# Kernel tuning notes

Measured on AMD Instinct MI355X. Metric: run time of the kernel, lower is better.

The kernel has to match this reference:

```python
import jax, jax.numpy as jnp
import numpy as np

EPS_COS = 1e-8   # torch cosine_similarity eps
EPS_SHARP = 1e-6 # sharpening normalizer eps
SHIFT_RANGE = 3
MEM_WIDTH = 64


def setup_inputs() -> dict:
    key = jax.random.key(0)
    k1, k2, k3, k4, k5 = jax.random.split(key, 5)
    B, H, N, W, D = 64, 4, 16384, MEM_WIDTH, 1024
    P = W + 6  # key(W) + beta + gate + shift(3) + gamma
    return {
        "controller_state": jax.random.normal(k1, (B, D), dtype=jnp.float32),
        "prev_weights": jax.random.uniform(k2, (B, H, N), dtype=jnp.float32),
        "memory": jax.random.normal(k3, (B, N, W), dtype=jnp.float32),
        "W_read": jax.random.normal(k4, (P * H, D), dtype=jnp.float32) * 0.02,
        "b_read": jax.random.normal(k5, (P * H,), dtype=jnp.float32) * 0.02,
    }


def reference(controller_state, prev_weights, memory, W_read, b_read):
    B, H, N = prev_weights.shape
    Wd = MEM_WIDTH
    # read head parameters: [B, H, P]
    params = (controller_state @ W_read.T + b_read).reshape(B, H, -1)
    key = params[..., :Wd]                                   # [B,H,W]
    beta = jax.nn.softplus(params[..., Wd])                  # [B,H]
    gate = jax.nn.sigmoid(params[..., Wd + 1])               # [B,H]
    shift = jax.nn.softmax(params[..., Wd + 2:Wd + 2 + SHIFT_RANGE], axis=-1)  # [B,H,3]
    gamma = 1.0 + jax.nn.softplus(params[..., Wd + 2 + SHIFT_RANGE])           # [B,H]

    # content addressing: cosine similarity of key vs each memory slot
    dots = jnp.einsum('bhw,bnw->bhn', key, memory)           # [B,H,N]
    key_norm = jnp.maximum(jnp.linalg.norm(key, axis=-1), EPS_COS)        # [B,H]
    mem_norm = jnp.maximum(jnp.linalg.norm(memory, axis=-1), EPS_COS)     # [B,N]
    sim = dots / (key_norm[:, :, None] * mem_norm[:, None, :])
    content_w = jax.nn.softmax(sim * beta[:, :, None], axis=-1)           # [B,H,N]

    # interpolate with previous weights
    g = gate[:, :, None]
    gated = g * content_w + (1.0 - g) * prev_weights                     # [B,H,N]

    # circular shift: out[pos] = s0*w[pos-1] + s1*w[pos] + s2*w[pos+1]
    shifted = (shift[..., 0:1] * jnp.roll(gated, 1, axis=-1)
               + shift[..., 1:2] * gated
               + shift[..., 2:3] * jnp.roll(gated, -1, axis=-1))

    # sharpening
    sharp = shifted ** gamma[:, :, None]
    sharp = sharp / (jnp.sum(sharp, axis=-1, keepdims=True) + EPS_SHARP)
    return sharp  # [B,H,N]
```

## Files before the change

kernel.cpp:

```cpp
#include <hip/hip_runtime.h>
#include <math.h>

#define B  64
#define H  4
#define NN 16384
#define WD 64
#define DD 1024
#define PP 70

typedef float fx4 __attribute__((ext_vector_type(4)));

__device__ __forceinline__ float softplus_f(float x) {
    return fmaxf(x, 0.f) + log1pf(expf(-fabsf(x)));
}

__global__ __launch_bounds__(256) void k_params(
    const float* __restrict__ state, const float* __restrict__ Wr,
    const float* __restrict__ br, float* __restrict__ kscaled,
    float* __restrict__ coef)
{
    int bh = blockIdx.x;
    int b  = bh >> 2, h = bh & 3;
    int tid = threadIdx.x, wave = tid >> 6, lane = tid & 63;
    __shared__ float sp[PP];
    __shared__ float sbc[1];

    const float4* st4 = (const float4*)(state + (size_t)b * DD);
    for (int j = wave; j < PP; j += 4) {
        const float4* w4 = (const float4*)(Wr + (size_t)(h * PP + j) * DD);
        float acc = 0.f;
        #pragma unroll
        for (int q = 0; q < 4; ++q) {
            float4 wv = w4[lane + 64 * q];
            float4 sv = st4[lane + 64 * q];
            acc += wv.x * sv.x + wv.y * sv.y + wv.z * sv.z + wv.w * sv.w;
        }
        #pragma unroll
        for (int m = 32; m >= 1; m >>= 1) acc += __shfl_xor(acc, m, 64);
        if (lane == 0) sp[j] = acc + br[h * PP + j];
    }
    __syncthreads();
    if (tid == 0) {
        float ss = 0.f;
        for (int w = 0; w < WD; ++w) ss += sp[w] * sp[w];
        float knorm = fmaxf(sqrtf(ss), 1e-8f);
        float beta  = softplus_f(sp[64]);
        float gate  = 1.f / (1.f + expf(-sp[65]));
        float m3 = fmaxf(sp[66], fmaxf(sp[67], sp[68]));
        float e0 = expf(sp[66] - m3), e1 = expf(sp[67] - m3), e2 = expf(sp[68] - m3);
        float es = e0 + e1 + e2;
        float gamma = 1.f + softplus_f(sp[69]);
        float* c = coef + bh * 8;
        c[0] = gate; c[1] = e0 / es; c[2] = e1 / es; c[3] = e2 / es; c[4] = gamma;
        sbc[0] = beta / knorm;
    }
    __syncthreads();
    if (tid < WD) kscaled[bh * WD + tid] = sp[tid] * sbc[0];
}

__global__ __launch_bounds__(256) void k_sim(
    const float* __restrict__ mem, const float* __restrict__ kscaled,
    float* __restrict__ sbuf)
{
    int tid = threadIdx.x, wave = tid >> 6, lane = tid & 63;
    int blk = blockIdx.x;
    int b = blk >> 8;
    int nblk = (blk & 255) * 64;
    int r = lane >> 3, c = lane & 7;

    const float* ksb = kscaled + b * 4 * WD + c * 8;
    float4 k0a = *(const float4*)(ksb + 0 * WD);
    float4 k0b = *(const float4*)(ksb + 0 * WD + 4);
    float4 k1a = *(const float4*)(ksb + 1 * WD);
    float4 k1b = *(const float4*)(ksb + 1 * WD + 4);
    float4 k2a = *(const float4*)(ksb + 2 * WD);
    float4 k2b = *(const float4*)(ksb + 2 * WD + 4);
    float4 k3a = *(const float4*)(ksb + 3 * WD);
    float4 k3b = *(const float4*)(ksb + 3 * WD + 4);

    int nw = nblk + wave * 16;
    #pragma unroll
    for (int it = 0; it < 2; ++it) {
        int n = nw + it * 8 + r;
        const fx4* rp = (const fx4*)(mem + ((size_t)b * NN + n) * WD + c * 8);
        fx4 v0 = __builtin_nontemporal_load(rp);
        fx4 v1 = __builtin_nontemporal_load(rp + 1);
        float d0 = v0.x*k0a.x + v0.y*k0a.y + v0.z*k0a.z + v0.w*k0a.w
                 + v1.x*k0b.x + v1.y*k0b.y + v1.z*k0b.z + v1.w*k0b.w;
        float d1 = v0.x*k1a.x + v0.y*k1a.y + v0.z*k1a.z + v0.w*k1a.w
                 + v1.x*k1b.x + v1.y*k1b.y + v1.z*k1b.z + v1.w*k1b.w;
        float d2 = v0.x*k2a.x + v0.y*k2a.y + v0.z*k2a.z + v0.w*k2a.w
                 + v1.x*k2b.x + v1.y*k2b.y + v1.z*k2b.z + v1.w*k2b.w;
        float d3 = v0.x*k3a.x + v0.y*k3a.y + v0.z*k3a.z + v0.w*k3a.w
                 + v1.x*k3b.x + v1.y*k3b.y + v1.z*k3b.z + v1.w*k3b.w;
        float q  = v0.x*v0.x + v0.y*v0.y + v0.z*v0.z + v0.w*v0.w
                 + v1.x*v1.x + v1.y*v1.y + v1.z*v1.z + v1.w*v1.w;
        #pragma unroll
        for (int m = 1; m < 8; m <<= 1) {
            d0 += __shfl_xor(d0, m, 64);
            d1 += __shfl_xor(d1, m, 64);
            d2 += __shfl_xor(d2, m, 64);
            d3 += __shfl_xor(d3, m, 64);
            q  += __shfl_xor(q,  m, 64);
        }
        if (c < 4) {
            float mn = fmaxf(sqrtf(q), 1e-8f);
            float d  = (c == 0) ? d0 : ((c == 1) ? d1 : ((c == 2) ? d2 : d3));
            sbuf[((size_t)(b * 4 + c)) * NN + n] = d / mn;
        }
    }
}

__global__ __launch_bounds__(1024) void k_head(
    const float* __restrict__ sbuf, const float* __restrict__ prev,
    const float* __restrict__ coef, float* __restrict__ out)
{
    __shared__ float lds[NN];
    int bh = blockIdx.x;
    int tid = threadIdx.x, wave = tid >> 6, lane = tid & 63;
    const float* srow = sbuf + (size_t)bh * NN;
    const float* prow = prev + (size_t)bh * NN;
    float* orow = out + (size_t)bh * NN;
    const float* c = coef + bh * 8;
    float gate = c[0], sh0 = c[1], sh1 = c[2], sh2 = c[3], gamma = c[4];

    float sv[16], pw[16];
    #pragma unroll
    for (int k = 0; k < 16; ++k) {
        sv[k] = srow[tid + k * 1024];
        pw[k] = prow[tid + k * 1024];
    }
    float m = sv[0];
    #pragma unroll
    for (int k = 1; k < 16; ++k) m = fmaxf(m, sv[k]);
    #pragma unroll
    for (int d = 32; d >= 1; d >>= 1) m = fmaxf(m, __shfl_xor(m, d, 64));
    if (lane == 0) lds[wave] = m;
    __syncthreads();
    if (tid == 0) {
        float x = lds[0];
        for (int i = 1; i < 16; ++i) x = fmaxf(x, lds[i]);
        lds[16] = x;
    }
    __syncthreads();
    m = lds[16];
    __syncthreads();
    float ls = 0.f;
    #pragma unroll
    for (int k = 0; k < 16; ++k) { sv[k] = expf(sv[k] - m); ls += sv[k]; }
    #pragma unroll
    for (int d = 32; d >= 1; d >>= 1) ls += __shfl_xor(ls, d, 64);
    if (lane == 0) lds[wave] = ls;
    __syncthreads();
    if (tid == 0) {
        float x = 0.f;
        for (int i = 0; i < 16; ++i) x += lds[i];
        lds[16] = x;
    }
    __syncthreads();
    float S = lds[16];
    __syncthreads();
    #pragma unroll
    for (int k = 0; k < 16; ++k) {
        float cw = sv[k] / S;
        lds[tid + k * 1024] = gate * cw + (1.f - gate) * pw[k];
    }
    __syncthreads();
    float sh[16];
    float ps = 0.f;
    #pragma unroll
    for (int k = 0; k < 16; ++k) {
        int n = tid + k * 1024;
        float gm1 = lds[(n + NN - 1) & (NN - 1)];
        float g0  = lds[n];
        float gp1 = lds[(n + 1) & (NN - 1)];
        float val = sh0 * gm1 + sh1 * g0 + sh2 * gp1;
        sh[k] = powf(val, gamma);
        ps += sh[k];
    }
    __syncthreads();
    #pragma unroll
    for (int d = 32; d >= 1; d >>= 1) ps += __shfl_xor(ps, d, 64);
    if (lane == 0) lds[wave] = ps;
    __syncthreads();
    if (tid == 0) {
        float x = 0.f;
        for (int i = 0; i < 16; ++i) x += lds[i];
        lds[16] = x;
    }
    __syncthreads();
    float T = lds[16] + 1e-6f;
    #pragma unroll
    for (int k = 0; k < 16; ++k) orow[tid + k * 1024] = sh[k] / T;
}

extern "C" void kernel_launch(void* const* d_in, const int* in_sizes, int n_in,
                              void* d_out, int out_size, void* d_ws, size_t ws_size,
                              hipStream_t stream) {
    const float* state = (const float*)d_in[0];
    const float* prev  = (const float*)d_in[1];
    const float* mem   = (const float*)d_in[2];
    const float* Wr    = (const float*)d_in[3];
    const float* br    = (const float*)d_in[4];
    float* out = (float*)d_out;

    float* sbuf    = (float*)d_ws;
    float* kscaled = sbuf + (size_t)B * H * NN;
    float* coef    = kscaled + (size_t)B * H * WD;

    k_params<<<B * H, 256, 0, stream>>>(state, Wr, br, kscaled, coef);
    k_sim<<<(B * NN) / 64, 256, 0, stream>>>(mem, kscaled, sbuf);
    k_head<<<B * H, 1024, 0, stream>>>(sbuf, prev, coef, out);
}
```

Before: 413.9 us.

## Fuse softmax exp and sum into similarity kernel using beta as max bound

The similarity kernel now computes exp(sim*beta - beta) directly, using the fact that cosine similarity is at most 1 so beta bounds the maximum. It writes the exponentials and accumulates per-head sums with atomics, which removes the max and sum reduction passes and their block barriers from the head kernel. The sharpening power is also replaced by fast exp/log intrinsics, and the final divide by a reciprocal multiply. The cost is nondeterministic float atomic summation and lower-precision fast math intrinsics.

```diff
diff --git a/kernel.cpp b/kernel.cpp
--- a/kernel.cpp
+++ b/kernel.cpp
@@ -17,7 +17,7 @@
 __global__ __launch_bounds__(256) void k_params(
     const float* __restrict__ state, const float* __restrict__ Wr,
     const float* __restrict__ br, float* __restrict__ kscaled,
-    float* __restrict__ coef)
+    float* __restrict__ coef, float* __restrict__ sums)
 {
     int bh = blockIdx.x;
     int b  = bh >> 2, h = bh & 3;
@@ -51,7 +51,9 @@
         float es = e0 + e1 + e2;
         float gamma = 1.f + softplus_f(sp[69]);
         float* c = coef + bh * 8;
-        c[0] = gate; c[1] = e0 / es; c[2] = e1 / es; c[3] = e2 / es; c[4] = gamma;
+        c[0] = gate; c[1] = e0 / es; c[2] = e1 / es; c[3] = e2 / es;
+        c[4] = gamma; c[5] = beta;
+        sums[bh] = 0.f;
         sbc[0] = beta / knorm;
     }
     __syncthreads();
@@ -60,7 +62,8 @@
 
 __global__ __launch_bounds__(256) void k_sim(
     const float* __restrict__ mem, const float* __restrict__ kscaled,
-    float* __restrict__ sbuf)
+    const float* __restrict__ coef, float* __restrict__ ebuf,
+    float* __restrict__ sums)
 {
     int tid = threadIdx.x, wave = tid >> 6, lane = tid & 63;
     int blk = blockIdx.x;
@@ -77,6 +80,9 @@
     float4 k2b = *(const float4*)(ksb + 2 * WD + 4);
     float4 k3a = *(const float4*)(ksb + 3 * WD);
     float4 k3b = *(const float4*)(ksb + 3 * WD + 4);
+
+    float bet = (c < 4) ? coef[(b * 4 + c) * 8 + 5] : 0.f;
+    float psum = 0.f;
 
     int nw = nblk + wave * 16;
     #pragma unroll
@@ -106,64 +112,36 @@
         if (c < 4) {
             float mn = fmaxf(sqrtf(q), 1e-8f);
             float d  = (c == 0) ? d0 : ((c == 1) ? d1 : ((c == 2) ? d2 : d3));
-            sbuf[((size_t)(b * 4 + c)) * NN + n] = d / mn;
+            float e  = __expf(d / mn - bet);
+            ebuf[((size_t)(b * 4 + c)) * NN + n] = e;
+            psum += e;
         }
     }
+    #pragma unroll
+    for (int m = 8; m < 64; m <<= 1) psum += __shfl_xor(psum, m, 64);
+    if (r == 0 && c < 4) atomicAdd(&sums[b * 4 + c], psum);
 }
 
 __global__ __launch_bounds__(1024) void k_head(
-    const float* __restrict__ sbuf, const float* __restrict__ prev,
-    const float* __restrict__ coef, float* __restrict__ out)
+    const float* __restrict__ ebuf, const float* __restrict__ prev,
+    const float* __restrict__ coef, const float* __restrict__ sums,
+    float* __restrict__ out)
 {
     __shared__ float lds[NN];
     int bh = blockIdx.x;
     int tid = threadIdx.x, wave = tid >> 6, lane = tid & 63;
-    const float* srow = sbuf + (size_t)bh * NN;
+    const float* erow = ebuf + (size_t)bh * NN;
     const float* prow = prev + (size_t)bh * NN;
     float* orow = out + (size_t)bh * NN;
     const float* c = coef + bh * 8;
     float gate = c[0], sh0 = c[1], sh1 = c[2], sh2 = c[3], gamma = c[4];
+    float ginvS = gate / sums[bh];
+    float omg   = 1.f - gate;
 
-    float sv[16], pw[16];
     #pragma unroll
     for (int k = 0; k < 16; ++k) {
-        sv[k] = srow[tid + k * 1024];
-        pw[k] = prow[tid + k * 1024];
-    }
-    float m = sv[0];
-    #pragma unroll
-    for (int k = 1; k < 16; ++k) m = fmaxf(m, sv[k]);
-    #pragma unroll
-    for (int d = 32; d >= 1; d >>= 1) m = fmaxf(m, __shfl_xor(m, d, 64));
-    if (lane == 0) lds[wave] = m;
-    __syncthreads();
-    if (tid == 0) {
-        float x = lds[0];
-        for (int i = 1; i < 16; ++i) x = fmaxf(x, lds[i]);
-        lds[16] = x;
-    }
-    __syncthreads();
-    m = lds[16];
-    __syncthreads();
-    float ls = 0.f;
-    #pragma unroll
-    for (int k = 0; k < 16; ++k) { sv[k] = expf(sv[k] - m); ls += sv[k]; }
-    #pragma unroll
-    for (int d = 32; d >= 1; d >>= 1) ls += __shfl_xor(ls, d, 64);
-    if (lane == 0) lds[wave] = ls;
-    __syncthreads();
-    if (tid == 0) {
-        float x = 0.f;
-        for (int i = 0; i < 16; ++i) x += lds[i];
-        lds[16] = x;
-    }
-    __syncthreads();
-    float S = lds[16];
-    __syncthreads();
-    #pragma unroll
-    for (int k = 0; k < 16; ++k) {
-        float cw = sv[k] / S;
-        lds[tid + k * 1024] = gate * cw + (1.f - gate) * pw[k];
+        int n = tid + k * 1024;
+        lds[n] = ginvS * erow[n] + omg * prow[n];
     }
     __syncthreads();
     float sh[16];
@@ -175,7 +153,7 @@
         float g0  = lds[n];
         float gp1 = lds[(n + 1) & (NN - 1)];
         float val = sh0 * gm1 + sh1 * g0 + sh2 * gp1;
-        sh[k] = powf(val, gamma);
+        sh[k] = __expf(gamma * __logf(val));
         ps += sh[k];
     }
     __syncthreads();
@@ -190,8 +168,9 @@
     }
     __syncthreads();
     float T = lds[16] + 1e-6f;
+    float invT = 1.f / T;
     #pragma unroll
-    for (int k = 0; k < 16; ++k) orow[tid + k * 1024] = sh[k] / T;
+    for (int k = 0; k < 16; ++k) orow[tid + k * 1024] = sh[k] * invT;
 }
 
 extern "C" void kernel_launch(void* const* d_in, const int* in_sizes, int n_in,
@@ -204,11 +183,12 @@
     const float* br    = (const float*)d_in[4];
     float* out = (float*)d_out;
 
-    float* sbuf    = (float*)d_ws;
-    float* kscaled = sbuf + (size_t)B * H * NN;
+    float* ebuf    = (float*)d_ws;
+    float* kscaled = ebuf + (size_t)B * H * NN;
     float* coef    = kscaled + (size_t)B * H * WD;
+    float* sums    = coef + (size_t)B * H * 8;
 
-    k_params<<<B * H, 256, 0, stream>>>(state, Wr, br, kscaled, coef);
-    k_sim<<<(B * NN) / 64, 256, 0, stream>>>(mem, kscaled, sbuf);
-    k_head<<<B * H, 1024, 0, stream>>>(sbuf, prev, coef, out);
+    k_params<<<B * H, 256, 0, stream>>>(state, Wr, br, kscaled, coef, sums);
+    k_sim<<<(B * NN) / 64, 256, 0, stream>>>(mem, kscaled, coef, ebuf, sums);
+    k_head<<<B * H, 1024, 0, stream>>>(ebuf, prev, coef, sums, out);
 }
```

Measured after the change: 601.8 us. 1.45x slower.
